# Performance work log

Measured on AMD Instinct MI355X. Metric: run time of the kernel, lower is better.

Reference implementation:

```python
import jax, jax.numpy as jnp
import numpy as np

B, N, C, H = 4, 1024, 768, 12
D = C // H  # head_dim = 64


def setup_inputs() -> dict:
    key = jax.random.key(0)
    ks = jax.random.split(key, 16)
    def lin(k, fan_in, fan_out):
        # torch Linear init: U(-1/sqrt(fan_in), 1/sqrt(fan_in)); stored as [in, out]
        bound = 1.0 / np.sqrt(fan_in)
        kw, kb = jax.random.split(k)
        W = jax.random.uniform(kw, (fan_in, fan_out), minval=-bound, maxval=bound, dtype=jnp.float32)
        b = jax.random.uniform(kb, (fan_out,), minval=-bound, maxval=bound, dtype=jnp.float32)
        return W, b
    Wq, bq = lin(ks[0], C, C)
    Wk, bk = lin(ks[1], C, C)
    Wv, bv = lin(ks[2], C, C)
    Wo, bo = lin(ks[3], C, C)
    Wd1, bd1 = lin(ks[4], 1, 16)
    Wd2, bd2 = lin(ks[5], 16, H)
    x = jax.random.normal(ks[6], (B, N, C), dtype=jnp.float32)
    coords = jax.random.uniform(ks[7], (B, N, 2), dtype=jnp.float32)
    return {"x": x, "coords": coords,
            "Wq": Wq, "bq": bq, "Wk": Wk, "bk": bk, "Wv": Wv, "bv": bv,
            "Wo": Wo, "bo": bo, "Wd1": Wd1, "bd1": bd1, "Wd2": Wd2, "bd2": bd2}


def reference(x, coords, Wq, bq, Wk, bk, Wv, bv, Wo, bo, Wd1, bd1, Wd2, bd2):
    scale = D ** (-0.5)
    # projections -> [B, H, N, D]
    def heads(t):
        return t.reshape(B, N, H, D).transpose(0, 2, 1, 3)
    q = heads(x @ Wq + bq)
    k = heads(x @ Wk + bk)
    v = heads(x @ Wv + bv)
    # content scores [B, H, N, N]
    content = jnp.einsum('bhid,bhjd->bhij', q, k) * scale
    # pairwise distances [B, N, N, 1]
    diff = coords[:, :, None, :] - coords[:, None, :, :]
    dist = jnp.sqrt(jnp.sum(diff * diff, axis=-1, keepdims=True) + 1e-6)
    # distance MLP: 1 -> 16 -> H, then permute to [B, H, N, N]
    hbias = jax.nn.relu(dist @ Wd1 + bd1)
    spatial = (hbias @ Wd2 + bd2).transpose(0, 3, 1, 2)
    attn = jax.nn.softmax(content + spatial, axis=-1)
    out = jnp.einsum('bhij,bhjd->bhid', attn, v)
    out = out.transpose(0, 2, 1, 3).reshape(B, N, C)
    out = out @ Wo + bo
    return out, attn
```

## Files before the change

kernel.cpp:

```cpp
#include <hip/hip_runtime.h>
#include <cstddef>
#include <cstdint>

#define Bc 4
#define Nc 1024
#define Cc 768
#define Hc 12
#define Dc 64
#define BHc 48
#define QKV_ELEMS ((size_t)Bc * Nc * Cc)

typedef __attribute__((ext_vector_type(4))) unsigned int u32x4;
typedef __attribute__((ext_vector_type(8))) short s16x8;
typedef __attribute__((ext_vector_type(8))) _Float16 h16x8;
typedef __attribute__((ext_vector_type(4))) unsigned short u16x4;
typedef __attribute__((ext_vector_type(4))) float fx4;
typedef __attribute__((ext_vector_type(2))) float fx2;

union Frag { u32x4 u; s16x8 s; h16x8 f16; unsigned short h[8]; };
union Half4 { u16x4 q; _Float16 h[4]; };

__device__ inline unsigned short f2bf(float x) {
    union { float f; uint32_t u; } c; c.f = x;
    return (unsigned short)((c.u + 0x7FFFu + ((c.u >> 16) & 1u)) >> 16);
}
__device__ inline float bf2f(unsigned short b) {
    union { uint32_t u; float f; } c; c.u = ((uint32_t)b) << 16;
    return c.f;
}
__device__ inline void split8(const float* v, u32x4& hi, u32x4& lo) {
    Frag fh, fl;
    #pragma unroll
    for (int e = 0; e < 8; ++e) {
        const unsigned short hb = f2bf(v[e]);
        fh.h[e] = hb;
        fl.h[e] = f2bf(v[e] - bf2f(hb));
    }
    hi = fh.u; lo = fl.u;
}
__device__ inline void split8h(const float* v, u32x4& hi, u32x4& lo) {
    Frag fh, fl;
    #pragma unroll
    for (int e = 0; e < 8; ++e) {
        const _Float16 hb = (_Float16)v[e];
        fh.f16[e] = hb;
        fl.f16[e] = (_Float16)(v[e] - (float)hb);
    }
    hi = fh.u; lo = fl.u;
}

__global__ __launch_bounds__(256) void prep_w_kernel(
    const float* __restrict__ Wq, const float* __restrict__ Wk,
    const float* __restrict__ Wv, const float* __restrict__ Wo,
    unsigned short* __restrict__ Thi, unsigned short* __restrict__ Tlo)
{
    __shared__ float scr[64 * 65];
    const int mat = blockIdx.z;
    const float* W = (mat == 0) ? Wq : (mat == 1) ? Wk : (mat == 2) ? Wv : Wo;
    const int k0 = blockIdx.y * 64, n0 = blockIdx.x * 64;
    const int tid = threadIdx.x;

    #pragma unroll
    for (int it = 0; it < 4; ++it) {
        const int lin = tid + it * 256;
        const int r = lin >> 4, c4 = (lin & 15) << 2;
        const fx4 v = *(const fx4*)&W[(size_t)(k0 + r) * 768 + n0 + c4];
        scr[r * 65 + c4 + 0] = v[0]; scr[r * 65 + c4 + 1] = v[1];
        scr[r * 65 + c4 + 2] = v[2]; scr[r * 65 + c4 + 3] = v[3];
    }
    __syncthreads();
    unsigned short* th = Thi + (size_t)mat * 768 * 768;
    unsigned short* tl = Tlo + (size_t)mat * 768 * 768;
    #pragma unroll
    for (int it = 0; it < 16; ++it) {
        const int lin = tid + it * 256;
        const int n = lin >> 6, kq = lin & 63;
        const float val = scr[kq * 65 + n];
        const size_t o = (size_t)(n0 + n) * 768 + k0 + kq;
        const unsigned short hb = f2bf(val);
        th[o] = hb;
        tl[o] = f2bf(val - bf2f(hb));
    }
}

__global__ __launch_bounds__(256) void prep_tables_kernel(
    const float* __restrict__ Wd1, const float* __restrict__ bd1,
    const float* __restrict__ Wd2, const float* __restrict__ bd2,
    float* __restrict__ abPack, unsigned char* __restrict__ lut)
{
    __shared__ float w1s[16], b1s[16], kn[16];
    __shared__ int rank[16];
    const int tid = threadIdx.x;
    if (tid < 16) {
        const float w1 = Wd1[tid], b1 = bd1[tid];
        w1s[tid] = w1; b1s[tid] = b1;
        kn[tid] = (w1 != 0.0f) ? (-b1 / w1) : INFINITY;
    }
    __syncthreads();
    if (tid < 16) {
        int rk = 0;
        for (int u = 0; u < 16; ++u) {
            const float ku = kn[u], km = kn[tid];
            if (ku < km || (ku == km && u < tid)) ++rk;
        }
        rank[tid] = rk;
    }
    __syncthreads();
    if (tid < 17 * 12) {
        const int s = tid / 12, h = tid % 12;
        float a = 0.0f, be = bd2[h];
        for (int u = 0; u < 16; ++u) {
            const float w1 = w1s[u], b1 = b1s[u];
            bool act;
            if (w1 > 0.0f)      act = (rank[u] < s);
            else if (w1 < 0.0f) act = (rank[u] >= s);
            else                act = (b1 > 0.0f);
            if (act) {
                const float w2 = Wd2[u * 12 + h];
                a  += w2 * w1;
                be += w2 * b1;
            }
        }
        abPack[tid * 2 + 0] = a;
        abPack[tid * 2 + 1] = be;
    }
    for (int b = tid; b < 2048; b += 256) {
        const float rep = (b + 0.5f) * (1.41422f / 2048.0f);
        int cnt = 0;
        for (int t = 0; t < 16; ++t) cnt += (rep > kn[t]) ? 1 : 0;
        lut[b] = (unsigned char)cnt;
    }
}

__global__ __launch_bounds__(256) void split_x_kernel(
    const float* __restrict__ x, unsigned short* __restrict__ xhi,
    unsigned short* __restrict__ xlo)
{
    const size_t t = (size_t)blockIdx.x * 256 + threadIdx.x;
    float vv[8];
    const fx4 a = *(const fx4*)&x[t * 8];
    const fx4 b = *(const fx4*)&x[t * 8 + 4];
    vv[0]=a[0]; vv[1]=a[1]; vv[2]=a[2]; vv[3]=a[3];
    vv[4]=b[0]; vv[5]=b[1]; vv[6]=b[2]; vv[7]=b[3];
    u32x4 hi, lo; split8(vv, hi, lo);
    *(u32x4*)&xhi[t * 8] = hi;
    *(u32x4*)&xlo[t * 8] = lo;
}

struct SmemG { u32x4 ah[512]; u32x4 al[512]; u32x4 bh[512]; u32x4 bl[512]; };
struct SmemT { float scr[64 * 68]; };
union SmemU { SmemG g; SmemT t; };

template<int OMODE>
__global__ __launch_bounds__(256) void gemm_mfma_kernel(
    const unsigned short* __restrict__ Ahi, const unsigned short* __restrict__ Alo,
    const unsigned short* __restrict__ Bhi, const unsigned short* __restrict__ Blo,
    const float* __restrict__ bias,
    float* __restrict__ outF,
    unsigned short* __restrict__ Ohi, unsigned short* __restrict__ Olo)
{
    __shared__ SmemU sm;
    const int tid = threadIdx.x;
    const int w = tid >> 6, L = tid & 63;
    const int Lr = L & 15, Lg = L >> 4;
    const int m0 = blockIdx.y * 64, n0 = blockIdx.x * 64;

    fx4 acc[2][2] = {};

    for (int kk = 0; kk < 768; kk += 64) {
        #pragma unroll
        for (int it = 0; it < 2; ++it) {
            const int slot = tid + it * 256;
            const int s = slot >> 6, l = slot & 63;
            const int row = m0 + ((s >> 1) << 4) + (l & 15);
            const int kb = kk + ((s & 1) << 5) + ((l >> 4) << 3);
            sm.g.ah[slot] = *(const u32x4*)&Ahi[(size_t)row * 768 + kb];
            sm.g.al[slot] = *(const u32x4*)&Alo[(size_t)row * 768 + kb];
            const int col = n0 + ((s >> 1) << 4) + (l & 15);
            sm.g.bh[slot] = *(const u32x4*)&Bhi[(size_t)col * 768 + kb];
            sm.g.bl[slot] = *(const u32x4*)&Blo[(size_t)col * 768 + kb];
        }
        __syncthreads();
        #pragma unroll
        for (int kc = 0; kc < 2; ++kc) {
            Frag ah[2], al[2], bh[2], bl[2];
            #pragma unroll
            for (int mm = 0; mm < 2; ++mm) {
                const int rg = (w >> 1) * 2 + mm;
                ah[mm].u = sm.g.ah[(rg * 2 + kc) * 64 + L];
                al[mm].u = sm.g.al[(rg * 2 + kc) * 64 + L];
            }
            #pragma unroll
            for (int nn = 0; nn < 2; ++nn) {
                const int cg = (w & 1) * 2 + nn;
                bh[nn].u = sm.g.bh[(cg * 2 + kc) * 64 + L];
                bl[nn].u = sm.g.bl[(cg * 2 + kc) * 64 + L];
            }
            #pragma unroll
            for (int mm = 0; mm < 2; ++mm)
                #pragma unroll
                for (int nn = 0; nn < 2; ++nn) {
                    acc[mm][nn] = __builtin_amdgcn_mfma_f32_16x16x32_bf16(ah[mm].s, bh[nn].s, acc[mm][nn], 0, 0, 0);
                    acc[mm][nn] = __builtin_amdgcn_mfma_f32_16x16x32_bf16(ah[mm].s, bl[nn].s, acc[mm][nn], 0, 0, 0);
                    acc[mm][nn] = __builtin_amdgcn_mfma_f32_16x16x32_bf16(al[mm].s, bh[nn].s, acc[mm][nn], 0, 0, 0);
                }
        }
        __syncthreads();
    }

    #pragma unroll
    for (int mm = 0; mm < 2; ++mm) {
        const int rl = (w >> 1) * 32 + mm * 16 + Lg * 4;
        #pragma unroll
        for (int nn = 0; nn < 2; ++nn) {
            const int cl = (w & 1) * 32 + nn * 16 + Lr;
            const float bs = bias[n0 + cl];
            #pragma unroll
            for (int r = 0; r < 4; ++r)
                sm.t.scr[(rl + r) * 68 + cl] = acc[mm][nn][r] + bs;
        }
    }
    __syncthreads();

    if (OMODE == 0) {
        const int h = n0 >> 6;
        #pragma unroll
        for (int it = 0; it < 2; ++it) {
            const int t = tid + it * 256;
            const int r = t >> 3, d0 = (t & 7) << 3;
            float vv[8];
            #pragma unroll
            for (int e = 0; e < 8; ++e) vv[e] = sm.t.scr[r * 68 + d0 + e];
            u32x4 hi, lo; split8(vv, hi, lo);
            const int rg = m0 + r, b = rg >> 10, nloc = rg & 1023;
            const size_t o = (((size_t)(b * Hc + h) * Nc + nloc) << 6) + d0;
            *(u32x4*)&Ohi[o] = hi;
            *(u32x4*)&Olo[o] = lo;
        }
    } else if (OMODE == 1) {
        const int b = m0 >> 10, h = n0 >> 6, nbase = m0 & 1023;
        #pragma unroll
        for (int it = 0; it < 2; ++it) {
            const int t = tid + it * 256;
            const int dd = t >> 3, j0 = (t & 7) << 3;
            float vv[8];
            #pragma unroll
            for (int e = 0; e < 8; ++e) vv[e] = sm.t.scr[(j0 + e) * 68 + dd];
            u32x4 hi, lo; split8h(vv, hi, lo);
            const size_t o = (size_t)((b * Hc + h) * Dc + dd) * Nc + nbase + j0;
            *(u32x4*)&Ohi[o] = hi;
            *(u32x4*)&Olo[o] = lo;
        }
    } else {
        #pragma unroll
        for (int it = 0; it < 4; ++it) {
            const int lin = tid + it * 256;
            const int r = lin >> 4, c4 = (lin & 15) << 2;
            const fx4 v = *(const fx4*)&sm.t.scr[r * 68 + c4];
            *(fx4*)&outF[(size_t)(m0 + r) * 768 + n0 + c4] = v;
        }
    }
}

__global__ __launch_bounds__(256) void scores_kernel(
    const unsigned short* __restrict__ qhi, const unsigned short* __restrict__ qlo,
    const unsigned short* __restrict__ khi, const unsigned short* __restrict__ klo,
    const float* __restrict__ coords,
    const float* __restrict__ abPack, const unsigned char* __restrict__ lutg,
    unsigned short* __restrict__ e_ws, float* __restrict__ mlf)
{
    __shared__ fx2 abt[17];
    __shared__ unsigned char luts[2048];
    __shared__ fx2 cjs[512];

    const int tid = threadIdx.x;
    const int w = tid >> 6, L = tid & 63;
    const int Lr = L & 15, Lg = L >> 4;
    const int bh = blockIdx.z, b = bh / Hc, h = bh % Hc;
    const int i0 = blockIdx.x * 64, half = blockIdx.y;
    const int i = i0 + w * 16 + Lr;
    const int Lg4 = Lg * 4;

    if (tid < 17) abt[tid] = ((const fx2*)abPack)[tid * Hc + h];
    for (int t = tid; t < 512; t += 256) {
        ((uint32_t*)luts)[t] = ((const uint32_t*)lutg)[t];
        cjs[t] = *(const fx2*)&coords[((size_t)b * Nc + half * 512 + t) * 2];
    }

    Frag qh[2], ql[2];
    #pragma unroll
    for (int kc = 0; kc < 2; ++kc) {
        const size_t o = ((size_t)bh * Nc + i) * 64 + kc * 32 + Lg * 8;
        qh[kc].u = *(const u32x4*)&qhi[o];
        ql[kc].u = *(const u32x4*)&qlo[o];
    }
    const fx2 ci = *(const fx2*)&coords[((size_t)b * Nc + i) * 2];
    __syncthreads();

    const size_t mlbase = ((size_t)bh * Nc + i) * 16 + half * 8;

    for (int jt = 0; jt < 8; ++jt) {
        const int jbase = half * 512 + jt * 64;
        const int jtg = half * 8 + jt;

        fx4 acc[4] = {};
        #pragma unroll
        for (int kc = 0; kc < 2; ++kc) {
            Frag kh[4], kl[4];
            #pragma unroll
            for (int cg = 0; cg < 4; ++cg) {
                const size_t o = ((size_t)bh * Nc + jbase + cg * 16 + Lr) * 64 + kc * 32 + Lg * 8;
                kh[cg].u = *(const u32x4*)&khi[o];
                kl[cg].u = *(const u32x4*)&klo[o];
            }
            #pragma unroll
            for (int cg = 0; cg < 4; ++cg) {
                acc[cg] = __builtin_amdgcn_mfma_f32_16x16x32_bf16(kh[cg].s, qh[kc].s, acc[cg], 0, 0, 0);
                acc[cg] = __builtin_amdgcn_mfma_f32_16x16x32_bf16(kl[cg].s, qh[kc].s, acc[cg], 0, 0, 0);
                acc[cg] = __builtin_amdgcn_mfma_f32_16x16x32_bf16(kh[cg].s, ql[kc].s, acc[cg], 0, 0, 0);
            }
        }

        float sv[16];
        #pragma unroll
        for (int cg = 0; cg < 4; ++cg) {
            #pragma unroll
            for (int r = 0; r < 4; ++r) {
                const fx2 cj = cjs[jt * 64 + cg * 16 + Lg4 + r + (half * 512 == jbase - jt * 64 ? 0 : 0)];
                const float dx = ci[0] - cj[0], dy = ci[1] - cj[1];
                const float dist = sqrtf(fmaf(dx, dx, fmaf(dy, dy, 1e-6f)));
                int bin = (int)(dist * (2048.0f / 1.41422f));
                bin = (bin > 2047) ? 2047 : bin;
                const fx2 ab = abt[luts[bin]];
                sv[cg * 4 + r] = fmaf(acc[cg][r], 0.125f, fmaf(ab[0], dist, ab[1]));
            }
        }

        float tm = sv[0];
        #pragma unroll
        for (int e = 1; e < 16; ++e) tm = fmaxf(tm, sv[e]);
        tm = fmaxf(tm, __shfl_xor(tm, 16));
        tm = fmaxf(tm, __shfl_xor(tm, 32));

        float ts = 0.f;
        #pragma unroll
        for (int e = 0; e < 16; ++e) { sv[e] = __expf(sv[e] - tm); ts += sv[e]; }

        const size_t eT = (((size_t)bh * 16 + jtg) << 16);
        #pragma unroll
        for (int cg = 0; cg < 4; ++cg) {
            Half4 hs;
            #pragma unroll
            for (int r = 0; r < 4; ++r) hs.h[r] = (_Float16)sv[cg * 4 + r];
            const int kc = cg >> 1;
            const int Lgp = (cg & 1) * 2 + (Lg >> 1);
            const size_t eoff = eT + (size_t)kc * 32768 + (size_t)i * 32 + Lgp * 8 + (Lg & 1) * 4;
            *(u16x4*)&e_ws[eoff] = hs.q;
        }

        ts += __shfl_xor(ts, 16);
        ts += __shfl_xor(ts, 32);
        if (Lg == 0) {
            *(fx2*)&mlf[(mlbase + jt) * 2] = fx2{tm, ts};
        }
    }
}

union PvSmem {
    struct { u32x4 vh[512]; u32x4 vl[512]; } v;
    float scr[64 * 68];
};

__global__ __launch_bounds__(256) void pv_kernel(
    const unsigned short* __restrict__ e_ws,
    const unsigned short* __restrict__ vThi, const unsigned short* __restrict__ vTlo,
    const float* __restrict__ mlf,
    float* __restrict__ attn,
    unsigned short* __restrict__ Hphi, unsigned short* __restrict__ Hplo)
{
    __shared__ PvSmem sm;
    const int tid = threadIdx.x;
    const int w = tid >> 6, L = tid & 63;
    const int Lr = L & 15, Lg = L >> 4;
    const int bh = blockIdx.y, b = bh / Hc, h = bh % Hc;
    const int i0 = blockIdx.x * 64;
    const int i = i0 + w * 16 + Lr;

    const float* mlr = &mlf[((size_t)bh * Nc + i) * 32];
    float mt[16], lt[16];
    #pragma unroll
    for (int t = 0; t < 8; ++t) {
        const fx4 v = *(const fx4*)&mlr[t * 4];
        mt[t*2+0] = v[0]; lt[t*2+0] = v[1];
        mt[t*2+1] = v[2]; lt[t*2+1] = v[3];
    }
    float m_row = mt[0];
    #pragma unroll
    for (int t = 1; t < 16; ++t) m_row = fmaxf(m_row, mt[t]);
    float l_row = 0.f;
    #pragma unroll
    for (int t = 0; t < 16; ++t) l_row = fmaf(lt[t], __expf(mt[t] - m_row), l_row);
    const float il = 1.0f / l_row;

    fx4 acc[4] = {};
    const size_t arow = ((size_t)bh * Nc + i) * Nc;

    #pragma unroll
    for (int jt = 0; jt < 16; ++jt) {
        const int jbase = jt * 64;
        #pragma unroll
        for (int it = 0; it < 2; ++it) {
            const int s = tid + it * 256;
            const int l = s & 63;
            const int dd = ((s >> 7) << 4) + (l & 15);
            const int jo = jbase + ((s >> 6) & 1) * 32 + ((l >> 4) << 3);
            const size_t off = ((size_t)bh * Dc + dd) * Nc + jo;
            sm.v.vh[s] = *(const u32x4*)&vThi[off];
            sm.v.vl[s] = *(const u32x4*)&vTlo[off];
        }
        __syncthreads();

        const float f = __expf(mt[jt] - m_row) * il;
        const _Float16 fh = (_Float16)f;
        const size_t eT = (((size_t)bh * 16 + jt) << 16) + (size_t)i * 32 + Lg * 8;

        #pragma unroll
        for (int kc = 0; kc < 2; ++kc) {
            Frag ef;
            ef.u = *(const u32x4*)&e_ws[eT + kc * 32768];
            float pf[8];
            #pragma unroll
            for (int e = 0; e < 8; ++e) pf[e] = (float)ef.f16[e] * f;
            fx4 w0, w1;
            w0[0]=pf[0]; w0[1]=pf[1]; w0[2]=pf[2]; w0[3]=pf[3];
            w1[0]=pf[4]; w1[1]=pf[5]; w1[2]=pf[6]; w1[3]=pf[7];
            float* ap = &attn[arow + jbase + kc * 32 + Lg * 8];
            *(fx4*)ap = w0;
            *(fx4*)(ap + 4) = w1;
            Frag pa;
            pa.f16 = ef.f16 * fh;
            #pragma unroll
            for (int dg = 0; dg < 4; ++dg) {
                Frag vh, vl;
                vh.u = sm.v.vh[(dg * 2 + kc) * 64 + L];
                vl.u = sm.v.vl[(dg * 2 + kc) * 64 + L];
                acc[dg] = __builtin_amdgcn_mfma_f32_16x16x32_f16(pa.f16, vh.f16, acc[dg], 0, 0, 0);
                acc[dg] = __builtin_amdgcn_mfma_f32_16x16x32_f16(pa.f16, vl.f16, acc[dg], 0, 0, 0);
            }
        }
        __syncthreads();
    }

    #pragma unroll
    for (int dg = 0; dg < 4; ++dg)
        #pragma unroll
        for (int r = 0; r < 4; ++r)
            sm.scr[(w * 16 + Lg * 4 + r) * 68 + dg * 16 + Lr] = acc[dg][r];
    __syncthreads();

    #pragma unroll
    for (int it = 0; it < 2; ++it) {
        const int lin = tid + it * 256;
        const int row = lin >> 3, d0 = (lin & 7) << 3;
        float vv[8];
        #pragma unroll
        for (int e = 0; e < 8; ++e) vv[e] = sm.scr[row * 68 + d0 + e];
        u32x4 hi, lo; split8(vv, hi, lo);
        const size_t o = ((size_t)b * Nc + i0 + row) * Cc + h * Dc + d0;
        *(u32x4*)&Hphi[o] = hi;
        *(u32x4*)&Hplo[o] = lo;
    }
}

extern "C" void kernel_launch(void* const* d_in, const int* in_sizes, int n_in,
                              void* d_out, int out_size, void* d_ws, size_t ws_size,
                              hipStream_t stream)
{
    (void)in_sizes; (void)n_in; (void)out_size; (void)ws_size;

    const float* x      = (const float*)d_in[0];
    const float* coords = (const float*)d_in[1];
    const float* Wq = (const float*)d_in[2];  const float* bq = (const float*)d_in[3];
    const float* Wk = (const float*)d_in[4];  const float* bk = (const float*)d_in[5];
    const float* Wv = (const float*)d_in[6];  const float* bv = (const float*)d_in[7];
    const float* Wo = (const float*)d_in[8];  const float* bo = (const float*)d_in[9];
    const float* Wd1 = (const float*)d_in[10]; const float* bd1 = (const float*)d_in[11];
    const float* Wd2 = (const float*)d_in[12]; const float* bd2 = (const float*)d_in[13];

    float* out_main = (float*)d_out;
    float* attn     = out_main + QKV_ELEMS;

    uint8_t* wsb = (uint8_t*)d_ws;
    const size_t SZ_BF = (size_t)BHc * Nc * Dc * 2;
    const size_t SZ_W4 = (size_t)4 * 768 * 768 * 2;
    unsigned short* qhi  = (unsigned short*)(wsb + 0 * SZ_BF);
    unsigned short* qlo  = (unsigned short*)(wsb + 1 * SZ_BF);
    unsigned short* khi  = (unsigned short*)(wsb + 2 * SZ_BF);
    unsigned short* klo  = (unsigned short*)(wsb + 3 * SZ_BF);
    unsigned short* vThi = (unsigned short*)(wsb + 4 * SZ_BF);
    unsigned short* vTlo = (unsigned short*)(wsb + 5 * SZ_BF);
    unsigned short* xhi  = (unsigned short*)(wsb + 6 * SZ_BF);
    unsigned short* xlo  = (unsigned short*)(wsb + 7 * SZ_BF);
    unsigned short* Thi  = (unsigned short*)(wsb + 8 * SZ_BF);
    unsigned short* Tlo  = (unsigned short*)(wsb + 8 * SZ_BF + SZ_W4);
    float* mlbuf  = (float*)(wsb + 8 * SZ_BF + 2 * SZ_W4);
    float* abPack = mlbuf + (size_t)BHc * Nc * 32;
    unsigned char* lut = (unsigned char*)(abPack + 17 * 12 * 2);
    unsigned short* e_ws = (unsigned short*)(wsb + 8 * SZ_BF + 2 * SZ_W4
                              + (size_t)BHc * Nc * 32 * 4 + 8192);

    prep_w_kernel<<<dim3(12, 12, 4), 256, 0, stream>>>(Wq, Wk, Wv, Wo, Thi, Tlo);
    prep_tables_kernel<<<1, 256, 0, stream>>>(Wd1, bd1, Wd2, bd2, abPack, lut);
    split_x_kernel<<<dim3(1536), 256, 0, stream>>>(x, xhi, xlo);

    dim3 gGemm(12, 64);
    gemm_mfma_kernel<0><<<gGemm, 256, 0, stream>>>(
        xhi, xlo, Thi + (size_t)0 * 768 * 768, Tlo + (size_t)0 * 768 * 768,
        bq, nullptr, qhi, qlo);
    gemm_mfma_kernel<0><<<gGemm, 256, 0, stream>>>(
        xhi, xlo, Thi + (size_t)1 * 768 * 768, Tlo + (size_t)1 * 768 * 768,
        bk, nullptr, khi, klo);
    gemm_mfma_kernel<1><<<gGemm, 256, 0, stream>>>(
        xhi, xlo, Thi + (size_t)2 * 768 * 768, Tlo + (size_t)2 * 768 * 768,
        bv, nullptr, vThi, vTlo);

    scores_kernel<<<dim3(16, 2, 48), 256, 0, stream>>>(
        qhi, qlo, khi, klo, coords, abPack, lut, e_ws, mlbuf);

    pv_kernel<<<dim3(16, 48), 256, 0, stream>>>(
        e_ws, vThi, vTlo, mlbuf, attn, xhi, xlo);

    gemm_mfma_kernel<2><<<gGemm, 256, 0, stream>>>(
        xhi, xlo, Thi + (size_t)3 * 768 * 768, Tlo + (size_t)3 * 768 * 768,
        bo, out_main, nullptr, nullptr);
}
```

Measured before the change: 389.2 us.

## Fuse scores and PV kernels, keeping exp tiles in registers

Merges the score/softmax kernel and the PV kernel into one kernel per (row block, head). Exponentiated scores stay in registers as fp16 fragments and the running max/sum are combined online, so the large fp16 e workspace and the max/sum buffer are no longer written and re-read through global memory. Fragments are re-laid out through a swizzled LDS scratch buffer before the PV MFMAs. The cost is much higher register pressure (possible spills or lower occupancy) and half as many blocks as the old scores launch.

```diff
diff --git a/kernel.cpp b/kernel.cpp
--- a/kernel.cpp
+++ b/kernel.cpp
@@ -11,14 +11,13 @@
 #define QKV_ELEMS ((size_t)Bc * Nc * Cc)
 
 typedef __attribute__((ext_vector_type(4))) unsigned int u32x4;
+typedef __attribute__((ext_vector_type(2))) unsigned int u32x2;
 typedef __attribute__((ext_vector_type(8))) short s16x8;
 typedef __attribute__((ext_vector_type(8))) _Float16 h16x8;
-typedef __attribute__((ext_vector_type(4))) unsigned short u16x4;
 typedef __attribute__((ext_vector_type(4))) float fx4;
 typedef __attribute__((ext_vector_type(2))) float fx2;
 
 union Frag { u32x4 u; s16x8 s; h16x8 f16; unsigned short h[8]; };
-union Half4 { u16x4 q; _Float16 h[4]; };
 
 __device__ inline unsigned short f2bf(float x) {
     union { float f; uint32_t u; } c; c.f = x;
@@ -262,30 +261,41 @@
     }
 }
 
-__global__ __launch_bounds__(256) void scores_kernel(
+union PvSmem {
+    struct { u32x4 vh[512]; u32x4 vl[512]; } v;
+    float scr[64 * 68];
+};
+
+__global__ __launch_bounds__(256) void attn_fused_kernel(
     const unsigned short* __restrict__ qhi, const unsigned short* __restrict__ qlo,
     const unsigned short* __restrict__ khi, const unsigned short* __restrict__ klo,
+    const unsigned short* __restrict__ vThi, const unsigned short* __restrict__ vTlo,
     const float* __restrict__ coords,
     const float* __restrict__ abPack, const unsigned char* __restrict__ lutg,
-    unsigned short* __restrict__ e_ws, float* __restrict__ mlf)
+    float* __restrict__ attn,
+    unsigned short* __restrict__ Hphi, unsigned short* __restrict__ Hplo)
 {
+    __shared__ PvSmem sm;
+    __shared__ char escr[4 * 2048];
+    __shared__ fx2 cjs[1024];
+    __shared__ unsigned char luts[2048];
     __shared__ fx2 abt[17];
-    __shared__ unsigned char luts[2048];
-    __shared__ fx2 cjs[512];
 
     const int tid = threadIdx.x;
     const int w = tid >> 6, L = tid & 63;
     const int Lr = L & 15, Lg = L >> 4;
-    const int bh = blockIdx.z, b = bh / Hc, h = bh % Hc;
-    const int i0 = blockIdx.x * 64, half = blockIdx.y;
+    const int bh = blockIdx.y, b = bh / Hc, h = bh % Hc;
+    const int i0 = blockIdx.x * 64;
     const int i = i0 + w * 16 + Lr;
     const int Lg4 = Lg * 4;
 
     if (tid < 17) abt[tid] = ((const fx2*)abPack)[tid * Hc + h];
-    for (int t = tid; t < 512; t += 256) {
+    #pragma unroll
+    for (int t = tid; t < 512; t += 256)
         ((uint32_t*)luts)[t] = ((const uint32_t*)lutg)[t];
-        cjs[t] = *(const fx2*)&coords[((size_t)b * Nc + half * 512 + t) * 2];
-    }
+    #pragma unroll
+    for (int t = tid; t < 1024; t += 256)
+        cjs[t] = *(const fx2*)&coords[((size_t)b * Nc + t) * 2];
 
     Frag qh[2], ql[2];
     #pragma unroll
@@ -297,11 +307,13 @@
     const fx2 ci = *(const fx2*)&coords[((size_t)b * Nc + i) * 2];
     __syncthreads();
 
-    const size_t mlbase = ((size_t)bh * Nc + i) * 16 + half * 8;
-
-    for (int jt = 0; jt < 8; ++jt) {
-        const int jbase = half * 512 + jt * 64;
-        const int jtg = half * 8 + jt;
+    Frag ef[16][2];
+    float m_t[16];
+    float m_r = -INFINITY, l_r = 0.f;
+
+    #pragma unroll
+    for (int jt = 0; jt < 16; ++jt) {
+        const int jbase = jt * 64;
 
         fx4 acc[4] = {};
         #pragma unroll
@@ -326,7 +338,7 @@
         for (int cg = 0; cg < 4; ++cg) {
             #pragma unroll
             for (int r = 0; r < 4; ++r) {
-                const fx2 cj = cjs[jt * 64 + cg * 16 + Lg4 + r + (half * 512 == jbase - jt * 64 ? 0 : 0)];
+                const fx2 cj = cjs[jbase + cg * 16 + Lg4 + r];
                 const float dx = ci[0] - cj[0], dy = ci[1] - cj[1];
                 const float dist = sqrtf(fmaf(dx, dx, fmaf(dy, dy, 1e-6f)));
                 int bin = (int)(dist * (2048.0f / 1.41422f));
@@ -341,68 +353,35 @@
         for (int e = 1; e < 16; ++e) tm = fmaxf(tm, sv[e]);
         tm = fmaxf(tm, __shfl_xor(tm, 16));
         tm = fmaxf(tm, __shfl_xor(tm, 32));
+        m_t[jt] = tm;
 
         float ts = 0.f;
         #pragma unroll
         for (int e = 0; e < 16; ++e) { sv[e] = __expf(sv[e] - tm); ts += sv[e]; }
-
-        const size_t eT = (((size_t)bh * 16 + jtg) << 16);
-        #pragma unroll
-        for (int cg = 0; cg < 4; ++cg) {
-            Half4 hs;
-            #pragma unroll
-            for (int r = 0; r < 4; ++r) hs.h[r] = (_Float16)sv[cg * 4 + r];
-            const int kc = cg >> 1;
-            const int Lgp = (cg & 1) * 2 + (Lg >> 1);
-            const size_t eoff = eT + (size_t)kc * 32768 + (size_t)i * 32 + Lgp * 8 + (Lg & 1) * 4;
-            *(u16x4*)&e_ws[eoff] = hs.q;
-        }
-
         ts += __shfl_xor(ts, 16);
         ts += __shfl_xor(ts, 32);
-        if (Lg == 0) {
-            *(fx2*)&mlf[(mlbase + jt) * 2] = fx2{tm, ts};
-        }
-    }
-}
-
-union PvSmem {
-    struct { u32x4 vh[512]; u32x4 vl[512]; } v;
-    float scr[64 * 68];
-};
-
-__global__ __launch_bounds__(256) void pv_kernel(
-    const unsigned short* __restrict__ e_ws,
-    const unsigned short* __restrict__ vThi, const unsigned short* __restrict__ vTlo,
-    const float* __restrict__ mlf,
-    float* __restrict__ attn,
-    unsigned short* __restrict__ Hphi, unsigned short* __restrict__ Hplo)
-{
-    __shared__ PvSmem sm;
-    const int tid = threadIdx.x;
-    const int w = tid >> 6, L = tid & 63;
-    const int Lr = L & 15, Lg = L >> 4;
-    const int bh = blockIdx.y, b = bh / Hc, h = bh % Hc;
-    const int i0 = blockIdx.x * 64;
-    const int i = i0 + w * 16 + Lr;
-
-    const float* mlr = &mlf[((size_t)bh * Nc + i) * 32];
-    float mt[16], lt[16];
-    #pragma unroll
-    for (int t = 0; t < 8; ++t) {
-        const fx4 v = *(const fx4*)&mlr[t * 4];
-        mt[t*2+0] = v[0]; lt[t*2+0] = v[1];
-        mt[t*2+1] = v[2]; lt[t*2+1] = v[3];
-    }
-    float m_row = mt[0];
-    #pragma unroll
-    for (int t = 1; t < 16; ++t) m_row = fmaxf(m_row, mt[t]);
-    float l_row = 0.f;
-    #pragma unroll
-    for (int t = 0; t < 16; ++t) l_row = fmaf(lt[t], __expf(mt[t] - m_row), l_row);
-    const float il = 1.0f / l_row;
-
-    fx4 acc[4] = {};
+
+        #pragma unroll
+        for (int p = 0; p < 2; ++p) {
+            Frag f;
+            #pragma unroll
+            for (int r = 0; r < 4; ++r) {
+                f.f16[r]     = (_Float16)sv[(2 * p) * 4 + r];
+                f.f16[4 + r] = (_Float16)sv[(2 * p + 1) * 4 + r];
+            }
+            ef[jt][p] = f;
+        }
+
+        const float mnew = fmaxf(m_r, tm);
+        l_r = l_r * __expf(m_r - mnew) + ts * __expf(tm - mnew);
+        m_r = mnew;
+    }
+
+    const float m_row = m_r;
+    const float il = 1.0f / l_r;
+
+    char* ebase = escr + w * 2048;
+    fx4 oacc[4] = {};
     const size_t arow = ((size_t)bh * Nc + i) * Nc;
 
     #pragma unroll
@@ -418,19 +397,30 @@
             sm.v.vh[s] = *(const u32x4*)&vThi[off];
             sm.v.vl[s] = *(const u32x4*)&vTlo[off];
         }
+
+        #pragma unroll
+        for (int p = 0; p < 2; ++p) {
+            const Frag f = ef[jt][p];
+            u32x2 lo2, hi2;
+            lo2[0] = f.u[0]; lo2[1] = f.u[1];
+            hi2[0] = f.u[2]; hi2[1] = f.u[3];
+            const int j0 = (2 * p) * 16 + Lg4;
+            const int j1 = (2 * p + 1) * 16 + Lg4;
+            *(u32x2*)(ebase + ((Lr * 128 + j0 * 2) ^ ((Lr & 7) << 4))) = lo2;
+            *(u32x2*)(ebase + ((Lr * 128 + j1 * 2) ^ ((Lr & 7) << 4))) = hi2;
+        }
         __syncthreads();
 
-        const float f = __expf(mt[jt] - m_row) * il;
-        const _Float16 fh = (_Float16)f;
-        const size_t eT = (((size_t)bh * 16 + jt) << 16) + (size_t)i * 32 + Lg * 8;
+        const float fscale = __expf(m_t[jt] - m_row) * il;
+        const _Float16 fh = (_Float16)fscale;
 
         #pragma unroll
         for (int kc = 0; kc < 2; ++kc) {
-            Frag ef;
-            ef.u = *(const u32x4*)&e_ws[eT + kc * 32768];
+            Frag eA;
+            eA.u = *(u32x4*)(ebase + ((Lr * 128 + (kc * 32 + Lg * 8) * 2) ^ ((Lr & 7) << 4)));
             float pf[8];
             #pragma unroll
-            for (int e = 0; e < 8; ++e) pf[e] = (float)ef.f16[e] * f;
+            for (int e = 0; e < 8; ++e) pf[e] = (float)eA.f16[e] * fscale;
             fx4 w0, w1;
             w0[0]=pf[0]; w0[1]=pf[1]; w0[2]=pf[2]; w0[3]=pf[3];
             w1[0]=pf[4]; w1[1]=pf[5]; w1[2]=pf[6]; w1[3]=pf[7];
@@ -438,14 +428,14 @@
             *(fx4*)ap = w0;
             *(fx4*)(ap + 4) = w1;
             Frag pa;
-            pa.f16 = ef.f16 * fh;
+            pa.f16 = eA.f16 * fh;
             #pragma unroll
             for (int dg = 0; dg < 4; ++dg) {
                 Frag vh, vl;
                 vh.u = sm.v.vh[(dg * 2 + kc) * 64 + L];
                 vl.u = sm.v.vl[(dg * 2 + kc) * 64 + L];
-                acc[dg] = __builtin_amdgcn_mfma_f32_16x16x32_f16(pa.f16, vh.f16, acc[dg], 0, 0, 0);
-                acc[dg] = __builtin_amdgcn_mfma_f32_16x16x32_f16(pa.f16, vl.f16, acc[dg], 0, 0, 0);
+                oacc[dg] = __builtin_amdgcn_mfma_f32_16x16x32_f16(pa.f16, vh.f16, oacc[dg], 0, 0, 0);
+                oacc[dg] = __builtin_amdgcn_mfma_f32_16x16x32_f16(pa.f16, vl.f16, oacc[dg], 0, 0, 0);
             }
         }
         __syncthreads();
@@ -455,7 +445,7 @@
     for (int dg = 0; dg < 4; ++dg)
         #pragma unroll
         for (int r = 0; r < 4; ++r)
-            sm.scr[(w * 16 + Lg * 4 + r) * 68 + dg * 16 + Lr] = acc[dg][r];
+            sm.scr[(w * 16 + Lg * 4 + r) * 68 + dg * 16 + Lr] = oacc[dg][r];
     __syncthreads();
 
     #pragma unroll
@@ -503,11 +493,8 @@
     unsigned short* xlo  = (unsigned short*)(wsb + 7 * SZ_BF);
     unsigned short* Thi  = (unsigned short*)(wsb + 8 * SZ_BF);
     unsigned short* Tlo  = (unsigned short*)(wsb + 8 * SZ_BF + SZ_W4);
-    float* mlbuf  = (float*)(wsb + 8 * SZ_BF + 2 * SZ_W4);
-    float* abPack = mlbuf + (size_t)BHc * Nc * 32;
+    float* abPack = (float*)(wsb + 8 * SZ_BF + 2 * SZ_W4);
     unsigned char* lut = (unsigned char*)(abPack + 17 * 12 * 2);
-    unsigned short* e_ws = (unsigned short*)(wsb + 8 * SZ_BF + 2 * SZ_W4
-                              + (size_t)BHc * Nc * 32 * 4 + 8192);
 
     prep_w_kernel<<<dim3(12, 12, 4), 256, 0, stream>>>(Wq, Wk, Wv, Wo, Thi, Tlo);
     prep_tables_kernel<<<1, 256, 0, stream>>>(Wd1, bd1, Wd2, bd2, abPack, lut);
@@ -524,11 +511,9 @@
         xhi, xlo, Thi + (size_t)2 * 768 * 768, Tlo + (size_t)2 * 768 * 768,
         bv, nullptr, vThi, vTlo);
 
-    scores_kernel<<<dim3(16, 2, 48), 256, 0, stream>>>(
-        qhi, qlo, khi, klo, coords, abPack, lut, e_ws, mlbuf);
-
-    pv_kernel<<<dim3(16, 48), 256, 0, stream>>>(
-        e_ws, vThi, vTlo, mlbuf, attn, xhi, xlo);
+    attn_fused_kernel<<<dim3(16, 48), 256, 0, stream>>>(
+        qhi, qlo, khi, klo, vThi, vTlo, coords, abPack, lut,
+        attn, xhi, xlo);
 
     gemm_mfma_kernel<2><<<gGemm, 256, 0, stream>>>(
         xhi, xlo, Thi + (size_t)3 * 768 * 768, Tlo + (size_t)3 * 768 * 768,
```

Result: slower. 462.1 us (+18.7%).
